# Kernel tuning notes

Hardware: AMD Instinct MI355X
Metric: run time of the kernel (lower is better)

## Reference

```python
import jax, jax.numpy as jnp
import numpy as np

N_NODES = 50000
N_EDGES = 800000
FEAT_DIM = 16
HIDDEN = 128
N_LAYERS = 4
OUT_DIM = 12
N_GRAPHS = 1024

def setup_inputs() -> dict:
    key = jax.random.key(0)
    ks = jax.random.split(key, 8)
    return {
        "x": jax.random.normal(ks[0], (N_NODES, FEAT_DIM), jnp.float32),
        "edge_index": jax.random.randint(ks[1], (2, N_EDGES), 0, N_NODES, dtype=jnp.int32),
        "edge_attr": jnp.zeros((N_EDGES, 4), jnp.float32),
        "batch_idx": jnp.sort(jax.random.randint(ks[2], (N_NODES,), 0, N_GRAPHS, dtype=jnp.int32)),
        # node-embed MLP: Linear(16,128) -> relu -> Linear(128,128)
        "W_e1": jax.random.normal(ks[3], (FEAT_DIM, HIDDEN), jnp.float32) * 0.1,
        "b_e1": jnp.zeros((HIDDEN,), jnp.float32),
        "W_e2": jax.random.normal(ks[4], (HIDDEN, HIDDEN), jnp.float32) * 0.05,
        "b_e2": jnp.zeros((HIDDEN,), jnp.float32),
        # stacked GCNConv weights/biases for 4 layers
        "W_g": jax.random.normal(ks[5], (N_LAYERS, HIDDEN, HIDDEN), jnp.float32) * 0.05,
        "b_g": jnp.zeros((N_LAYERS, HIDDEN), jnp.float32),
        # output Linear(128,12)
        "W_o": jax.random.normal(ks[6], (HIDDEN, OUT_DIM), jnp.float32) * 0.05,
        "b_o": jnp.zeros((OUT_DIM,), jnp.float32),
    }

def _gcn_layer(h_in, src, dst, W, b):
    # PyG GCNConv with add_self_loops=True, symmetric normalization:
    # out_i = sum_{j in N(i) u {i}} (d_i d_j)^{-1/2} (x_j W) + b
    h = h_in @ W                                   # [N, H]
    deg = jnp.zeros((N_NODES,), h.dtype).at[dst].add(1.0) + 1.0  # +1 self-loop
    dinv = jax.lax.rsqrt(deg)                      # [N]
    norm = dinv[src] * dinv[dst]                   # [E]
    msg = h[src] * norm[:, None]                   # gather + scale  [E, H]
    agg = jnp.zeros_like(h).at[dst].add(msg)       # scatter-add to targets
    agg = agg + h * (dinv * dinv)[:, None]         # self-loop term
    return agg + b

def reference(x, edge_index, edge_attr, batch_idx, W_e1, b_e1, W_e2, b_e2, W_g, b_g, W_o, b_o):
    del edge_attr  # use_edge_attribution=False; GCNConv ignores edge features
    src, dst = edge_index[0], edge_index[1]
    # node embedding MLP
    h = jax.nn.relu(x @ W_e1 + b_e1) @ W_e2 + b_e2
    for i in range(N_LAYERS):
        h = jax.nn.relu(_gcn_layer(h, src, dst, W_g[i], b_g[i]))
        # dropout is identity in eval mode
    # scatter-mean pooling over graphs
    sums = jax.ops.segment_sum(h, batch_idx, num_segments=N_GRAPHS)
    cnts = jax.ops.segment_sum(jnp.ones((N_NODES,), h.dtype), batch_idx, num_segments=N_GRAPHS)
    pooled = sums / jnp.maximum(cnts, 1.0)[:, None]
    return pooled @ W_o + b_o
```

## Files before the change

### kernel.cpp

```cpp
#include <hip/hip_runtime.h>

#define N_NODES 50000
#define N_EDGES 800000
#define FEAT    16
#define HID     128
#define NLAYERS 4
#define OUTD    12
#define NGRAPH  1024
#define SCAN_NB 196

__device__ inline float4 f4zero() { return make_float4(0.f, 0.f, 0.f, 0.f); }
__device__ inline float4 f4fma(float a, float4 w, float4 acc) {
    acc.x = fmaf(a, w.x, acc.x);
    acc.y = fmaf(a, w.y, acc.y);
    acc.z = fmaf(a, w.z, acc.z);
    acc.w = fmaf(a, w.w, acc.w);
    return acc;
}
__device__ inline float4 f4add(float4 a, float4 b) {
    return make_float4(a.x + b.x, a.y + b.y, a.z + b.z, a.w + b.w);
}

__global__ void k_deg(const int* __restrict__ ei, int* __restrict__ degi) {
    int e = blockIdx.x * 256 + threadIdx.x;
    if (e < N_EDGES) atomicAdd(&degi[ei[N_EDGES + e]], 1);
}

__global__ void k_dinv(const int* __restrict__ degi, float* __restrict__ dinv) {
    int i = blockIdx.x * 256 + threadIdx.x;
    if (i < N_NODES) dinv[i] = rsqrtf((float)degi[i] + 1.0f);
}

__global__ void k_scan_part(const int* __restrict__ degi, int* __restrict__ part) {
    __shared__ int s[256];
    int t = threadIdx.x;
    int i = blockIdx.x * 256 + t;
    int v = (i < N_NODES) ? degi[i] : 0;
    s[t] = v;
    __syncthreads();
    for (int st = 128; st > 0; st >>= 1) {
        if (t < st) s[t] += s[t + st];
        __syncthreads();
    }
    if (t == 0) part[blockIdx.x] = s[0];
}

__global__ void k_scan_mid(int* __restrict__ part) {
    __shared__ int s[256];
    int t = threadIdx.x;
    int v = (t < SCAN_NB) ? part[t] : 0;
    s[t] = v;
    __syncthreads();
    for (int st = 1; st < 256; st <<= 1) {
        int u = (t >= st) ? s[t - st] : 0;
        __syncthreads();
        s[t] += u;
        __syncthreads();
    }
    if (t < SCAN_NB) part[t] = s[t] - v;
}

__global__ void k_scan_final(const int* __restrict__ degi, const int* __restrict__ part,
                             int* __restrict__ offs) {
    __shared__ int s[256];
    int t = threadIdx.x;
    int i = blockIdx.x * 256 + t;
    int v = (i < N_NODES) ? degi[i] : 0;
    s[t] = v;
    __syncthreads();
    for (int st = 1; st < 256; st <<= 1) {
        int u = (t >= st) ? s[t - st] : 0;
        __syncthreads();
        s[t] += u;
        __syncthreads();
    }
    if (i <= N_NODES) offs[i] = s[t] - v + part[blockIdx.x];
}

__global__ void k_fill(const int* __restrict__ ei, const int* __restrict__ offs,
                       const float* __restrict__ dinv,
                       int* __restrict__ cursor, int* __restrict__ csr,
                       float* __restrict__ csrnm) {
    int e = blockIdx.x * 256 + threadIdx.x;
    if (e < N_EDGES) {
        int srcv = ei[e];
        int dstv = ei[N_EDGES + e];
        int p = atomicAdd(&cursor[dstv], 1);
        int slot = offs[dstv] + p;
        csr[slot]   = srcv;
        csrnm[slot] = dinv[srcv];
    }
}

#define GM 32
__global__ void __launch_bounds__(256) k_embed1(
        const float* __restrict__ x,
        const float* __restrict__ W1, const float* __restrict__ b1,
        float* __restrict__ t_out) {
    __shared__ float x_l[GM][FEAT];
    int t = threadIdx.x;
    long n0 = (long)blockIdx.x * GM;
    if (t < 128) {
        int r  = t >> 2;
        int c4 = (t & 3) << 2;
        long n = n0 + r;
        float4 v = (n < N_NODES) ? *(const float4*)&x[n * FEAT + c4] : f4zero();
        *(float4*)&x_l[r][c4] = v;
    }
    __syncthreads();
    int fgrp = t & 31, ngrp = t >> 5;
    int f4 = fgrp << 2;
    float4 acc0 = f4zero(), acc1 = f4zero(), acc2 = f4zero(), acc3 = f4zero();
#pragma unroll
    for (int k = 0; k < FEAT; ++k) {
        float4 w = *(const float4*)&W1[k * HID + f4];
        acc0 = f4fma(x_l[ngrp * 4 + 0][k], w, acc0);
        acc1 = f4fma(x_l[ngrp * 4 + 1][k], w, acc1);
        acc2 = f4fma(x_l[ngrp * 4 + 2][k], w, acc2);
        acc3 = f4fma(x_l[ngrp * 4 + 3][k], w, acc3);
    }
    float4 bv = *(const float4*)&b1[f4];
    acc0 = f4add(acc0, bv); acc1 = f4add(acc1, bv);
    acc2 = f4add(acc2, bv); acc3 = f4add(acc3, bv);
    acc0.x = fmaxf(acc0.x, 0.f); acc0.y = fmaxf(acc0.y, 0.f); acc0.z = fmaxf(acc0.z, 0.f); acc0.w = fmaxf(acc0.w, 0.f);
    acc1.x = fmaxf(acc1.x, 0.f); acc1.y = fmaxf(acc1.y, 0.f); acc1.z = fmaxf(acc1.z, 0.f); acc1.w = fmaxf(acc1.w, 0.f);
    acc2.x = fmaxf(acc2.x, 0.f); acc2.y = fmaxf(acc2.y, 0.f); acc2.z = fmaxf(acc2.z, 0.f); acc2.w = fmaxf(acc2.w, 0.f);
    acc3.x = fmaxf(acc3.x, 0.f); acc3.y = fmaxf(acc3.y, 0.f); acc3.z = fmaxf(acc3.z, 0.f); acc3.w = fmaxf(acc3.w, 0.f);
    long n;
    n = n0 + ngrp * 4 + 0; if (n < N_NODES) *(float4*)&t_out[n * HID + f4] = acc0;
    n = n0 + ngrp * 4 + 1; if (n < N_NODES) *(float4*)&t_out[n * HID + f4] = acc1;
    n = n0 + ngrp * 4 + 2; if (n < N_NODES) *(float4*)&t_out[n * HID + f4] = acc2;
    n = n0 + ngrp * 4 + 3; if (n < N_NODES) *(float4*)&t_out[n * HID + f4] = acc3;
}

__global__ void __launch_bounds__(256) k_gemm(
        const float* __restrict__ A, const float* __restrict__ W,
        const float* __restrict__ bias, float* __restrict__ B) {
    __shared__ float a_l[GM][HID];
    int t = threadIdx.x;
    long n0 = (long)blockIdx.x * GM;
#pragma unroll
    for (int i = 0; i < 4; ++i) {
        int p  = t + 256 * i;
        int r  = p >> 5;
        int c4 = (p & 31) << 2;
        long n = n0 + r;
        float4 v = (n < N_NODES) ? *(const float4*)&A[n * HID + c4] : f4zero();
        *(float4*)&a_l[r][c4] = v;
    }
    __syncthreads();
    int fgrp = t & 31, ngrp = t >> 5;
    int f4 = fgrp << 2;
    float4 acc0 = f4zero(), acc1 = f4zero(), acc2 = f4zero(), acc3 = f4zero();
#pragma unroll 8
    for (int k = 0; k < HID; ++k) {
        float4 w = *(const float4*)&W[k * HID + f4];
        acc0 = f4fma(a_l[ngrp * 4 + 0][k], w, acc0);
        acc1 = f4fma(a_l[ngrp * 4 + 1][k], w, acc1);
        acc2 = f4fma(a_l[ngrp * 4 + 2][k], w, acc2);
        acc3 = f4fma(a_l[ngrp * 4 + 3][k], w, acc3);
    }
    if (bias) {
        float4 bv = *(const float4*)&bias[f4];
        acc0 = f4add(acc0, bv); acc1 = f4add(acc1, bv);
        acc2 = f4add(acc2, bv); acc3 = f4add(acc3, bv);
    }
    long n;
    n = n0 + ngrp * 4 + 0; if (n < N_NODES) *(float4*)&B[n * HID + f4] = acc0;
    n = n0 + ngrp * 4 + 1; if (n < N_NODES) *(float4*)&B[n * HID + f4] = acc1;
    n = n0 + ngrp * 4 + 2; if (n < N_NODES) *(float4*)&B[n * HID + f4] = acc2;
    n = n0 + ngrp * 4 + 3; if (n < N_NODES) *(float4*)&B[n * HID + f4] = acc3;
}

__global__ void __launch_bounds__(256) k_agg(
        const float* __restrict__ hp,
        const int* __restrict__ csr, const float* __restrict__ csrnm,
        const int* __restrict__ offs,
        const float* __restrict__ dinv, const float* __restrict__ bias,
        float* __restrict__ hout) {
    int t = threadIdx.x;
    int lane = t & 31, grp = t >> 5;
    int i = blockIdx.x * 8 + grp;
    if (i >= N_NODES) return;
    float di = dinv[i];
    int s0 = offs[i], s1 = offs[i + 1];
    const float4* hp4 = (const float4*)hp;
    float4 self = hp4[(long)i * 32 + lane];
    float4 acc  = *(const float4*)&bias[lane << 2];
    acc = f4fma(di * di, self, acc);
    for (int j = s0; j < s1; ++j) {
        int   sv = csr[j];
        float nm = di * csrnm[j];
        float4 v = hp4[(long)sv * 32 + lane];
        acc = f4fma(nm, v, acc);
    }
    acc.x = fmaxf(acc.x, 0.f); acc.y = fmaxf(acc.y, 0.f);
    acc.z = fmaxf(acc.z, 0.f); acc.w = fmaxf(acc.w, 0.f);
    ((float4*)hout)[(long)i * 32 + lane] = acc;
}

#define PN 16
__global__ void __launch_bounds__(256) k_pool(
        const float* __restrict__ h, const int* __restrict__ batch,
        float* __restrict__ pooled, float* __restrict__ cnt) {
    int t = threadIdx.x;
    int lane = t & 31, grp = t >> 5;
    long n0 = ((long)blockIdx.x * 8 + grp) * PN;
    if (n0 >= N_NODES) return;
    long n1 = n0 + PN; if (n1 > N_NODES) n1 = N_NODES;
    const float4* h4 = (const float4*)h;
    float4 run = f4zero();
    int curg = batch[n0];
    int c = 0;
    for (long n = n0; n < n1; ++n) {
        int g = batch[n];
        if (g != curg) {
            float* pb = &pooled[(long)curg * HID + (lane << 2)];
            atomicAdd(pb + 0, run.x); atomicAdd(pb + 1, run.y);
            atomicAdd(pb + 2, run.z); atomicAdd(pb + 3, run.w);
            if (lane == 0) atomicAdd(&cnt[curg], (float)c);
            run = f4zero(); c = 0; curg = g;
        }
        run = f4add(run, h4[n * 32 + lane]);
        ++c;
    }
    float* pb = &pooled[(long)curg * HID + (lane << 2)];
    atomicAdd(pb + 0, run.x); atomicAdd(pb + 1, run.y);
    atomicAdd(pb + 2, run.z); atomicAdd(pb + 3, run.w);
    if (lane == 0) atomicAdd(&cnt[curg], (float)c);
}

__global__ void __launch_bounds__(HID) k_out(
        const float* __restrict__ pooled, const float* __restrict__ cnt,
        const float* __restrict__ Wo, const float* __restrict__ bo,
        float* __restrict__ out) {
    __shared__ float p[HID];
    int g = blockIdx.x;
    int f = threadIdx.x;
    float inv = 1.0f / fmaxf(cnt[g], 1.0f);
    p[f] = pooled[g * HID + f] * inv;
    __syncthreads();
    if (f < OUTD) {
        float acc = bo[f];
#pragma unroll 8
        for (int k = 0; k < HID; ++k) acc += p[k] * Wo[k * OUTD + f];
        out[g * OUTD + f] = acc;
    }
}

extern "C" void kernel_launch(void* const* d_in, const int* in_sizes, int n_in,
                              void* d_out, int out_size, void* d_ws, size_t ws_size,
                              hipStream_t stream) {
    const float* x    = (const float*)d_in[0];
    const int*   ei   = (const int*)d_in[1];
    const int*   bidx = (const int*)d_in[3];
    const float* We1  = (const float*)d_in[4];
    const float* be1  = (const float*)d_in[5];
    const float* We2  = (const float*)d_in[6];
    const float* be2  = (const float*)d_in[7];
    const float* Wg   = (const float*)d_in[8];
    const float* bg   = (const float*)d_in[9];
    const float* Wo   = (const float*)d_in[10];
    const float* bo   = (const float*)d_in[11];
    float* out = (float*)d_out;

    char* ws = (char*)d_ws;
    size_t o = 0;
    auto take = [&](size_t bytes) { size_t r = o; o += (bytes + 255) & ~(size_t)255; return r; };
    size_t off_degi   = take((size_t)N_NODES * 4);
    size_t off_cursor = take((size_t)N_NODES * 4);
    size_t off_pooled = take((size_t)NGRAPH * HID * 4);
    size_t off_cnt    = take((size_t)NGRAPH * 4);
    size_t zero_bytes = o;
    size_t off_dinv   = take((size_t)N_NODES * 4);
    size_t off_offs   = take((size_t)(N_NODES + 1) * 4);
    size_t off_part   = take((size_t)256 * 4);
    size_t off_csr    = take((size_t)N_EDGES * 4);
    size_t off_csrnm  = take((size_t)N_EDGES * 4);
    size_t off_hA     = take((size_t)N_NODES * HID * 4);
    size_t off_hB     = take((size_t)N_NODES * HID * 4);

    int*   degi   = (int*)(ws + off_degi);
    int*   cursor = (int*)(ws + off_cursor);
    float* pooled = (float*)(ws + off_pooled);
    float* cnt    = (float*)(ws + off_cnt);
    float* dinv   = (float*)(ws + off_dinv);
    int*   offs   = (int*)(ws + off_offs);
    int*   part   = (int*)(ws + off_part);
    int*   csr    = (int*)(ws + off_csr);
    float* csrnm  = (float*)(ws + off_csrnm);
    float* hA     = (float*)(ws + off_hA);
    float* hB     = (float*)(ws + off_hB);

    hipMemsetAsync(d_ws, 0, zero_bytes, stream);

    k_deg<<<(N_EDGES + 255) / 256, 256, 0, stream>>>(ei, degi);
    k_dinv<<<(N_NODES + 255) / 256, 256, 0, stream>>>(degi, dinv);
    k_scan_part<<<SCAN_NB, 256, 0, stream>>>(degi, part);
    k_scan_mid<<<1, 256, 0, stream>>>(part);
    k_scan_final<<<SCAN_NB, 256, 0, stream>>>(degi, part, offs);
    k_fill<<<(N_EDGES + 255) / 256, 256, 0, stream>>>(ei, offs, dinv, cursor, csr, csrnm);

    int gemm_grid = (N_NODES + GM - 1) / GM;
    k_embed1<<<gemm_grid, 256, 0, stream>>>(x, We1, be1, hB);
    k_gemm<<<gemm_grid, 256, 0, stream>>>(hB, We2, be2, hA);

    for (int l = 0; l < NLAYERS; ++l) {
        k_gemm<<<gemm_grid, 256, 0, stream>>>(hA, Wg + (size_t)l * HID * HID, nullptr, hB);
        k_agg<<<(N_NODES + 7) / 8, 256, 0, stream>>>(hB, csr, csrnm, offs, dinv,
                                                     bg + (size_t)l * HID, hA);
    }

    k_pool<<<(N_NODES + 8 * PN - 1) / (8 * PN), 256, 0, stream>>>(hA, bidx, pooled, cnt);
    k_out<<<NGRAPH, HID, 0, stream>>>(pooled, cnt, Wo, bo, out);
}
```

Measured before the change: 647.3 us.

## Use wave64 per node in aggregation with shuffled edge batches; enlarge GEMM tile

The aggregation kernel now gives each node one full 64-lane wavefront, with each lane owning two features. Edge indices and norms are loaded cooperatively, 64 at a time, then broadcast with shuffles, and eight neighbor rows are gathered in flight before accumulating, which raises memory-level parallelism. Separately, the GEMM tile grows from 32 to 64 rows, so each thread holds 8 accumulators and reuses each weight load more. The costs are higher register pressure and more shared memory per GEMM block, fewer GEMM blocks, and wasted shuffle work on low-degree nodes.

```diff
diff --git a/kernel.cpp b/kernel.cpp
--- a/kernel.cpp
+++ b/kernel.cpp
@@ -92,14 +92,14 @@
     }
 }
 
-#define GM 32
+#define EM 32
 __global__ void __launch_bounds__(256) k_embed1(
         const float* __restrict__ x,
         const float* __restrict__ W1, const float* __restrict__ b1,
         float* __restrict__ t_out) {
-    __shared__ float x_l[GM][FEAT];
-    int t = threadIdx.x;
-    long n0 = (long)blockIdx.x * GM;
+    __shared__ float x_l[EM][FEAT];
+    int t = threadIdx.x;
+    long n0 = (long)blockIdx.x * EM;
     if (t < 128) {
         int r  = t >> 2;
         int c4 = (t & 3) << 2;
@@ -133,6 +133,7 @@
     n = n0 + ngrp * 4 + 3; if (n < N_NODES) *(float4*)&t_out[n * HID + f4] = acc3;
 }
 
+#define GM 64
 __global__ void __launch_bounds__(256) k_gemm(
         const float* __restrict__ A, const float* __restrict__ W,
         const float* __restrict__ bias, float* __restrict__ B) {
@@ -140,7 +141,7 @@
     int t = threadIdx.x;
     long n0 = (long)blockIdx.x * GM;
 #pragma unroll
-    for (int i = 0; i < 4; ++i) {
+    for (int i = 0; i < 8; ++i) {
         int p  = t + 256 * i;
         int r  = p >> 5;
         int c4 = (p & 31) << 2;
@@ -151,25 +152,26 @@
     __syncthreads();
     int fgrp = t & 31, ngrp = t >> 5;
     int f4 = fgrp << 2;
-    float4 acc0 = f4zero(), acc1 = f4zero(), acc2 = f4zero(), acc3 = f4zero();
+    float4 acc[8];
+#pragma unroll
+    for (int r = 0; r < 8; ++r) acc[r] = f4zero();
 #pragma unroll 8
     for (int k = 0; k < HID; ++k) {
         float4 w = *(const float4*)&W[k * HID + f4];
-        acc0 = f4fma(a_l[ngrp * 4 + 0][k], w, acc0);
-        acc1 = f4fma(a_l[ngrp * 4 + 1][k], w, acc1);
-        acc2 = f4fma(a_l[ngrp * 4 + 2][k], w, acc2);
-        acc3 = f4fma(a_l[ngrp * 4 + 3][k], w, acc3);
+#pragma unroll
+        for (int r = 0; r < 8; ++r)
+            acc[r] = f4fma(a_l[ngrp * 8 + r][k], w, acc[r]);
     }
     if (bias) {
         float4 bv = *(const float4*)&bias[f4];
-        acc0 = f4add(acc0, bv); acc1 = f4add(acc1, bv);
-        acc2 = f4add(acc2, bv); acc3 = f4add(acc3, bv);
-    }
-    long n;
-    n = n0 + ngrp * 4 + 0; if (n < N_NODES) *(float4*)&B[n * HID + f4] = acc0;
-    n = n0 + ngrp * 4 + 1; if (n < N_NODES) *(float4*)&B[n * HID + f4] = acc1;
-    n = n0 + ngrp * 4 + 2; if (n < N_NODES) *(float4*)&B[n * HID + f4] = acc2;
-    n = n0 + ngrp * 4 + 3; if (n < N_NODES) *(float4*)&B[n * HID + f4] = acc3;
+#pragma unroll
+        for (int r = 0; r < 8; ++r) acc[r] = f4add(acc[r], bv);
+    }
+#pragma unroll
+    for (int r = 0; r < 8; ++r) {
+        long n = n0 + ngrp * 8 + r;
+        if (n < N_NODES) *(float4*)&B[n * HID + f4] = acc[r];
+    }
 }
 
 __global__ void __launch_bounds__(256) k_agg(
@@ -179,24 +181,47 @@
         const float* __restrict__ dinv, const float* __restrict__ bias,
         float* __restrict__ hout) {
     int t = threadIdx.x;
-    int lane = t & 31, grp = t >> 5;
-    int i = blockIdx.x * 8 + grp;
+    int lane = t & 63;
+    int w = t >> 6;
+    int i = blockIdx.x * 4 + w;
     if (i >= N_NODES) return;
     float di = dinv[i];
     int s0 = offs[i], s1 = offs[i + 1];
-    const float4* hp4 = (const float4*)hp;
-    float4 self = hp4[(long)i * 32 + lane];
-    float4 acc  = *(const float4*)&bias[lane << 2];
-    acc = f4fma(di * di, self, acc);
-    for (int j = s0; j < s1; ++j) {
-        int   sv = csr[j];
-        float nm = di * csrnm[j];
-        float4 v = hp4[(long)sv * 32 + lane];
-        acc = f4fma(nm, v, acc);
-    }
-    acc.x = fmaxf(acc.x, 0.f); acc.y = fmaxf(acc.y, 0.f);
-    acc.z = fmaxf(acc.z, 0.f); acc.w = fmaxf(acc.w, 0.f);
-    ((float4*)hout)[(long)i * 32 + lane] = acc;
+    const float2* hp2 = (const float2*)hp;
+    float2 self = hp2[(long)i * 64 + lane];
+    float2 bv = ((const float2*)bias)[lane];
+    float ax = fmaf(di * di, self.x, bv.x);
+    float ay = fmaf(di * di, self.y, bv.y);
+    for (int base = s0; base < s1; base += 64) {
+        int n = s1 - base; if (n > 64) n = 64;
+        int last = n - 1;
+        int idx = base + lane;
+        int   sv_l = (lane < n) ? csr[idx]        : 0;
+        float nm_l = (lane < n) ? csrnm[idx] * di : 0.f;
+        for (int k = 0; k < n; k += 8) {
+            int a[8]; float m[8];
+#pragma unroll
+            for (int u = 0; u < 8; ++u) {
+                int kk = k + u;
+                int ks = kk < last ? kk : last;
+                a[u] = __shfl(sv_l, ks);
+                float mu = __shfl(nm_l, ks);
+                m[u] = (kk < n) ? mu : 0.f;
+            }
+            float2 v[8];
+#pragma unroll
+            for (int u = 0; u < 8; ++u) v[u] = hp2[(long)a[u] * 64 + lane];
+#pragma unroll
+            for (int u = 0; u < 8; ++u) {
+                ax = fmaf(m[u], v[u].x, ax);
+                ay = fmaf(m[u], v[u].y, ay);
+            }
+        }
+    }
+    float2 r;
+    r.x = fmaxf(ax, 0.f);
+    r.y = fmaxf(ay, 0.f);
+    ((float2*)hout)[(long)i * 64 + lane] = r;
 }
 
 #define PN 16
@@ -301,13 +326,13 @@
     k_scan_final<<<SCAN_NB, 256, 0, stream>>>(degi, part, offs);
     k_fill<<<(N_EDGES + 255) / 256, 256, 0, stream>>>(ei, offs, dinv, cursor, csr, csrnm);
 
+    k_embed1<<<(N_NODES + EM - 1) / EM, 256, 0, stream>>>(x, We1, be1, hB);
     int gemm_grid = (N_NODES + GM - 1) / GM;
-    k_embed1<<<gemm_grid, 256, 0, stream>>>(x, We1, be1, hB);
     k_gemm<<<gemm_grid, 256, 0, stream>>>(hB, We2, be2, hA);
 
     for (int l = 0; l < NLAYERS; ++l) {
         k_gemm<<<gemm_grid, 256, 0, stream>>>(hA, Wg + (size_t)l * HID * HID, nullptr, hB);
-        k_agg<<<(N_NODES + 7) / 8, 256, 0, stream>>>(hB, csr, csrnm, offs, dinv,
+        k_agg<<<(N_NODES + 3) / 4, 256, 0, stream>>>(hB, csr, csrnm, offs, dinv,
                                                      bg + (size_t)l * HID, hA);
     }
 
```

Measured after the change: 594.4 us. 1.09x faster.
